# Kernel optimization log

Measured on AMD Instinct MI355X. Metric: run time of the kernel, lower is better.

The kernel has to match this reference:

```python
import jax, jax.numpy as jnp
import numpy as np

N = 100000          # nodes
E = 1600000         # edges (avg degree 16)
D_IN = 128          # in_features
D_OUT = 128         # out_features


def setup_inputs() -> dict:
    key = jax.random.key(0)
    k1, k2, k3, k4 = jax.random.split(key, 4)
    H = jax.random.normal(k1, (N, D_IN), dtype=jnp.float32)
    # COO indices of sparse adjacency A: row i aggregates features of col j
    src = jax.random.randint(k2, (E,), 0, N, dtype=jnp.int32)
    dst = jax.random.randint(k3, (E,), 0, N, dtype=jnp.int32)
    # nn.Linear(2*in_features, out_features): weight [out, 2*in], zero bias
    W = jax.random.normal(k4, (D_OUT, 2 * D_IN), dtype=jnp.float32) * 0.05
    b = jnp.zeros((D_OUT,), dtype=jnp.float32)
    return {"H": H, "src": src, "dst": dst, "W": W, "b": b}


def reference(H, src, dst, W, b):
    # max-aggregation: for each node i, max over features of its neighbors.
    # One fused gather + segment-max replaces the per-node Python loop.
    gathered = H[dst]  # [E, D_IN]
    agg = jax.ops.segment_max(gathered, src, num_segments=N)  # [N, D_IN]
    # nodes with no incoming edges stay zero (torch code leaves zeros)
    deg = jax.ops.segment_sum(jnp.ones((src.shape[0],), jnp.float32), src,
                              num_segments=N)  # [N]
    H_neigh = jnp.where(deg[:, None] > 0, agg, 0.0)
    H_concat = jnp.concatenate([H, H_neigh], axis=1)  # [N, 2*D_IN]
    return H_concat @ W.T + b
```

## Files before the change

kernel.cpp:

```cpp
#include <hip/hip_runtime.h>
#include <math.h>

#define NN 100000
#define NE 1600000
#define DD 128
#define NB 1563
#define CAP 1280
#define PB 391
#define CB 391

#define WS_HH  0
#define WS_CUR 6400000
#define WS_ENT (WS_CUR + NB)
#define WS_AH  (WS_ENT + NB * CAP)

typedef __attribute__((ext_vector_type(8))) _Float16 h8_t;
typedef __attribute__((ext_vector_type(4))) _Float16 h4_t;
typedef __attribute__((ext_vector_type(2))) _Float16 h2_t;
typedef __attribute__((ext_vector_type(4))) float f4_t;

__device__ __forceinline__ unsigned pk2h(float x, float y) {
    h2_t h;
    h.x = (_Float16)x;
    h.y = (_Float16)y;
    return *(unsigned*)&h;
}

__device__ __forceinline__ h4_t h4max(h4_t a, h4_t b) {
    return __builtin_elementwise_max(a, b);
}

__global__ __launch_bounds__(512) void prep_kernel(const float* __restrict__ H,
                                                   const int* __restrict__ src,
                                                   const int* __restrict__ dst,
                                                   int* __restrict__ cursor,
                                                   unsigned* __restrict__ entries,
                                                   uint4* __restrict__ Hh4) {
    __shared__ int cnt[NB];
    __shared__ int gcur[NB];
    const int t = threadIdx.x;
    const int b = blockIdx.x;
    if (b < PB) {
        for (int i = t; i < NB; i += 512) cnt[i] = 0;
        __syncthreads();
        const int base = b * 4096;
        int sv[8];
#pragma unroll
        for (int k = 0; k < 8; ++k) {
            int e = base + k * 512 + t;
            sv[k] = (e < NE) ? src[e] : -1;
            if (sv[k] >= 0) atomicAdd(&cnt[sv[k] >> 6], 1);
        }
        __syncthreads();
        for (int i = t; i < NB; i += 512) {
            int c = cnt[i];
            gcur[i] = c ? i * CAP + atomicAdd(&cursor[i], c) : 0;
        }
        __syncthreads();
#pragma unroll
        for (int k = 0; k < 8; ++k) {
            int e = base + k * 512 + t;
            if (sv[k] >= 0) {
                int s = sv[k];
                int pos = atomicAdd(&gcur[s >> 6], 1);
                entries[pos] = ((unsigned)(s & 63) << 17) | (unsigned)dst[e];
            }
        }
    } else {
        const int nb = b - PB;
        const int n8 = NN * DD / 8;
        for (int i = nb * 512 + t; i < n8; i += CB * 512) {
            const float4* s = (const float4*)H + (size_t)i * 2;
            float4 a = s[0], c4 = s[1];
            uint4 o;
            o.x = pk2h(a.x, a.y);
            o.y = pk2h(a.z, a.w);
            o.z = pk2h(c4.x, c4.y);
            o.w = pk2h(c4.z, c4.w);
            Hh4[i] = o;
        }
    }
}

__global__ __launch_bounds__(256) void agg_kernel(const _Float16* __restrict__ Hh,
                                                  const int* __restrict__ cursor,
                                                  const unsigned* __restrict__ entries,
                                                  unsigned* __restrict__ Ah) {
    __shared__ unsigned raw[CAP];
    __shared__ unsigned sorted[CAP];
    __shared__ int cnt[64], base_s[64], cur[64];
    const int t = threadIdx.x;
    const int b = blockIdx.x;
    const int n = cursor[b];

    if (t < 64) cnt[t] = 0;
    __syncthreads();
    for (int i = t; i < n; i += 256) {
        unsigned e = entries[b * CAP + i];
        raw[i] = e;
        atomicAdd(&cnt[e >> 17], 1);
    }
    __syncthreads();
    if (t < 64) {
        int v = cnt[t];
        int incl = v;
#pragma unroll
        for (int o = 1; o < 64; o <<= 1) {
            int y = __shfl_up(incl, o, 64);
            if (t >= o) incl += y;
        }
        base_s[t] = incl - v;
        cur[t] = incl - v;
    }
    __syncthreads();
    for (int i = t; i < n; i += 256) {
        unsigned e = raw[i];
        int pos = atomicAdd(&cur[e >> 17], 1);
        sorted[pos] = e & 0x1FFFFu;
    }
    __syncthreads();

    const int lane = t & 63;
    const int w = t >> 6;
    const int half = lane >> 5;
    const int l32 = lane & 31;
    const _Float16* __restrict__ colbase = Hh + l32 * 4;
#pragma unroll
    for (int q = 0; q < 16; ++q) {
        int ln = w * 16 + q;
        int s0 = base_s[ln];
        int e0 = s0 + cnt[ln];
        unsigned long long mu = 0xFC00FC00FC00FC00ull;
        h4_t m = *(h4_t*)&mu;
        int j = s0 + half;
        for (; j + 6 < e0; j += 8) {
            int d0 = sorted[j], d1 = sorted[j + 2];
            int d2 = sorted[j + 4], d3 = sorted[j + 6];
            h4_t v0 = *(const h4_t*)(colbase + (size_t)d0 * DD);
            h4_t v1 = *(const h4_t*)(colbase + (size_t)d1 * DD);
            h4_t v2 = *(const h4_t*)(colbase + (size_t)d2 * DD);
            h4_t v3 = *(const h4_t*)(colbase + (size_t)d3 * DD);
            m = h4max(m, h4max(h4max(v0, v1), h4max(v2, v3)));
        }
        for (; j < e0; j += 2) {
            h4_t v0 = *(const h4_t*)(colbase + (size_t)sorted[j] * DD);
            m = h4max(m, v0);
        }
        uint2 mv = *(uint2*)&m;
        uint2 ov;
        ov.x = (unsigned)__shfl_xor((int)mv.x, 32, 64);
        ov.y = (unsigned)__shfl_xor((int)mv.y, 32, 64);
        h4_t om = *(h4_t*)&ov;
        m = h4max(m, om);
        int node = b * 64 + ln;
        if (half == 0 && node < NN) {
            uint2 outv = make_uint2(0u, 0u);
            if (s0 < e0) outv = *(uint2*)&m;
            *(uint2*)(Ah + (size_t)node * 64 + l32 * 2) = outv;
        }
    }
}

#define XP 72
__global__ __launch_bounds__(256) void mfma_matmul_kernel(
        const unsigned short* __restrict__ Hh,
        const unsigned short* __restrict__ Ah,
        const float* __restrict__ W,
        const float* __restrict__ bias,
        float* __restrict__ out) {
    __shared__ unsigned short Xs[64 * XP];
    __shared__ unsigned short Ws[128 * XP];
    const int t = threadIdx.x;
    const int lane = t & 63;
    const int w = t >> 6;
    const int quad = lane >> 4;
    const int l16 = lane & 15;
    const int blockrow = blockIdx.x * 64;

    f4_t acc[8] = {};

    for (int c = 0; c < 4; ++c) {
        const int k0 = c * 64;
        {
            const unsigned short* xb = (c < 2) ? Hh : Ah;
            const int koff = (c < 2) ? k0 : k0 - 128;
            int seg = t & 7, r0 = t >> 3;
#pragma unroll
            for (int j = 0; j < 2; ++j) {
                int r = r0 + 32 * j;
                int row = blockrow + r;
                uint4 v = make_uint4(0, 0, 0, 0);
                if (row < NN)
                    v = *(const uint4*)(xb + (size_t)row * DD + koff + seg * 8);
                *(uint4*)&Xs[r * XP + seg * 8] = v;
            }
        }
        {
            int seg = t & 15, o0 = t >> 4;
#pragma unroll
            for (int j = 0; j < 8; ++j) {
                int o = o0 + 16 * j;
                float4 wv = *(const float4*)(W + (size_t)o * 256 + k0 + seg * 4);
                uint2 p;
                p.x = pk2h(wv.x, wv.y);
                p.y = pk2h(wv.z, wv.w);
                *(uint2*)&Ws[o * XP + seg * 4] = p;
            }
        }
        __syncthreads();
#pragma unroll
        for (int kk = 0; kk < 64; kk += 32) {
            h8_t a = *(const h8_t*)&Xs[(w * 16 + l16) * XP + kk + quad * 8];
#pragma unroll
            for (int ot = 0; ot < 8; ++ot) {
                h8_t bf = *(const h8_t*)&Ws[(ot * 16 + l16) * XP + kk + quad * 8];
                acc[ot] = __builtin_amdgcn_mfma_f32_16x16x32_f16(a, bf, acc[ot], 0, 0, 0);
            }
        }
        __syncthreads();
    }

#pragma unroll
    for (int ot = 0; ot < 8; ++ot) {
        float bv = bias[ot * 16 + l16];
#pragma unroll
        for (int reg = 0; reg < 4; ++reg) {
            int row = blockrow + w * 16 + quad * 4 + reg;
            if (row < NN)
                out[(size_t)row * DD + ot * 16 + l16] = acc[ot][reg] + bv;
        }
    }
}

extern "C" void kernel_launch(void* const* d_in, const int* in_sizes, int n_in,
                              void* d_out, int out_size, void* d_ws, size_t ws_size,
                              hipStream_t stream) {
    const float* H   = (const float*)d_in[0];
    const int*   src = (const int*)d_in[1];
    const int*   dst = (const int*)d_in[2];
    const float* W   = (const float*)d_in[3];
    const float* b   = (const float*)d_in[4];
    float* out = (float*)d_out;

    int* ws = (int*)d_ws;
    unsigned short* Hh      = (unsigned short*)(ws + WS_HH);
    int*            cursor  = ws + WS_CUR;
    unsigned*       entries = (unsigned*)(ws + WS_ENT);
    unsigned*       Ah      = (unsigned*)(ws + WS_AH);

    hipMemsetAsync(cursor, 0, NB * sizeof(int), stream);
    prep_kernel<<<PB + CB, 512, 0, stream>>>(H, src, dst, cursor, entries, (uint4*)Hh);
    agg_kernel<<<NB, 256, 0, stream>>>((const _Float16*)Hh, cursor, entries, Ah);
    mfma_matmul_kernel<<<(NN + 63) / 64, 256, 0, stream>>>(
        Hh, (const unsigned short*)Ah, W, b, out);
}
```

Before: 245.0 us.

## Pre-convert W to fp16 once, enlarge matmul row tile, widen prep blocks

```diff
diff --git a/kernel.cpp b/kernel.cpp
--- a/kernel.cpp
+++ b/kernel.cpp
@@ -6,13 +6,14 @@
 #define DD 128
 #define NB 1563
 #define CAP 1280
-#define PB 391
-#define CB 391
+#define PB 196
+#define CB 196
 
 #define WS_HH  0
 #define WS_CUR 6400000
 #define WS_ENT (WS_CUR + NB)
 #define WS_AH  (WS_ENT + NB * CAP)
+#define WS_WH  (WS_AH + NN * (DD / 2))
 
 typedef __attribute__((ext_vector_type(8))) _Float16 h8_t;
 typedef __attribute__((ext_vector_type(4))) _Float16 h4_t;
@@ -30,36 +31,45 @@
     return __builtin_elementwise_max(a, b);
 }
 
-__global__ __launch_bounds__(512) void prep_kernel(const float* __restrict__ H,
-                                                   const int* __restrict__ src,
-                                                   const int* __restrict__ dst,
-                                                   int* __restrict__ cursor,
-                                                   unsigned* __restrict__ entries,
-                                                   uint4* __restrict__ Hh4) {
+__global__ __launch_bounds__(1024) void init_kernel(const float* __restrict__ W,
+                                                    unsigned* __restrict__ Wh,
+                                                    int* __restrict__ cursor) {
+    int i = blockIdx.x * 1024 + threadIdx.x;
+    if (i < 128 * 256 / 2) Wh[i] = pk2h(W[2 * i], W[2 * i + 1]);
+    int j = i - 128 * 256 / 2;
+    if (j >= 0 && j < NB) cursor[j] = 0;
+}
+
+__global__ __launch_bounds__(1024) void prep_kernel(const float* __restrict__ H,
+                                                    const int* __restrict__ src,
+                                                    const int* __restrict__ dst,
+                                                    int* __restrict__ cursor,
+                                                    unsigned* __restrict__ entries,
+                                                    uint4* __restrict__ Hh4) {
     __shared__ int cnt[NB];
     __shared__ int gcur[NB];
     const int t = threadIdx.x;
     const int b = blockIdx.x;
     if (b < PB) {
-        for (int i = t; i < NB; i += 512) cnt[i] = 0;
-        __syncthreads();
-        const int base = b * 4096;
+        for (int i = t; i < NB; i += 1024) cnt[i] = 0;
+        __syncthreads();
+        const int base = b * 8192;
         int sv[8];
 #pragma unroll
         for (int k = 0; k < 8; ++k) {
-            int e = base + k * 512 + t;
+            int e = base + k * 1024 + t;
             sv[k] = (e < NE) ? src[e] : -1;
             if (sv[k] >= 0) atomicAdd(&cnt[sv[k] >> 6], 1);
         }
         __syncthreads();
-        for (int i = t; i < NB; i += 512) {
+        for (int i = t; i < NB; i += 1024) {
             int c = cnt[i];
             gcur[i] = c ? i * CAP + atomicAdd(&cursor[i], c) : 0;
         }
         __syncthreads();
 #pragma unroll
         for (int k = 0; k < 8; ++k) {
-            int e = base + k * 512 + t;
+            int e = base + k * 1024 + t;
             if (sv[k] >= 0) {
                 int s = sv[k];
                 int pos = atomicAdd(&gcur[s >> 6], 1);
@@ -69,7 +79,7 @@
     } else {
         const int nb = b - PB;
         const int n8 = NN * DD / 8;
-        for (int i = nb * 512 + t; i < n8; i += CB * 512) {
+        for (int i = nb * 1024 + t; i < n8; i += CB * 1024) {
             const float4* s = (const float4*)H + (size_t)i * 2;
             float4 a = s[0], c4 = s[1];
             uint4 o;
@@ -165,28 +175,28 @@
 __global__ __launch_bounds__(256) void mfma_matmul_kernel(
         const unsigned short* __restrict__ Hh,
         const unsigned short* __restrict__ Ah,
-        const float* __restrict__ W,
+        const unsigned short* __restrict__ Wh,
         const float* __restrict__ bias,
         float* __restrict__ out) {
-    __shared__ unsigned short Xs[64 * XP];
+    __shared__ unsigned short Xs[128 * XP];
     __shared__ unsigned short Ws[128 * XP];
     const int t = threadIdx.x;
     const int lane = t & 63;
     const int w = t >> 6;
     const int quad = lane >> 4;
     const int l16 = lane & 15;
-    const int blockrow = blockIdx.x * 64;
-
-    f4_t acc[8] = {};
+    const int blockrow = blockIdx.x * 128;
+
+    f4_t acc[2][8] = {};
 
     for (int c = 0; c < 4; ++c) {
         const int k0 = c * 64;
         {
             const unsigned short* xb = (c < 2) ? Hh : Ah;
             const int koff = (c < 2) ? k0 : k0 - 128;
-            int seg = t & 7, r0 = t >> 3;
-#pragma unroll
-            for (int j = 0; j < 2; ++j) {
+            const int seg = t & 7, r0 = t >> 3;
+#pragma unroll
+            for (int j = 0; j < 4; ++j) {
                 int r = r0 + 32 * j;
                 int row = blockrow + r;
                 uint4 v = make_uint4(0, 0, 0, 0);
@@ -196,25 +206,24 @@
             }
         }
         {
-            int seg = t & 15, o0 = t >> 4;
-#pragma unroll
-            for (int j = 0; j < 8; ++j) {
-                int o = o0 + 16 * j;
-                float4 wv = *(const float4*)(W + (size_t)o * 256 + k0 + seg * 4);
-                uint2 p;
-                p.x = pk2h(wv.x, wv.y);
-                p.y = pk2h(wv.z, wv.w);
-                *(uint2*)&Ws[o * XP + seg * 4] = p;
+            const int seg = t & 7, o0 = t >> 3;
+#pragma unroll
+            for (int j = 0; j < 4; ++j) {
+                int o = o0 + 32 * j;
+                uint4 v = *(const uint4*)(Wh + (size_t)o * 256 + k0 + seg * 8);
+                *(uint4*)&Ws[o * XP + seg * 8] = v;
             }
         }
         __syncthreads();
 #pragma unroll
         for (int kk = 0; kk < 64; kk += 32) {
-            h8_t a = *(const h8_t*)&Xs[(w * 16 + l16) * XP + kk + quad * 8];
+            h8_t a0 = *(const h8_t*)&Xs[(w * 32 + l16) * XP + kk + quad * 8];
+            h8_t a1 = *(const h8_t*)&Xs[(w * 32 + 16 + l16) * XP + kk + quad * 8];
 #pragma unroll
             for (int ot = 0; ot < 8; ++ot) {
                 h8_t bf = *(const h8_t*)&Ws[(ot * 16 + l16) * XP + kk + quad * 8];
-                acc[ot] = __builtin_amdgcn_mfma_f32_16x16x32_f16(a, bf, acc[ot], 0, 0, 0);
+                acc[0][ot] = __builtin_amdgcn_mfma_f32_16x16x32_f16(a0, bf, acc[0][ot], 0, 0, 0);
+                acc[1][ot] = __builtin_amdgcn_mfma_f32_16x16x32_f16(a1, bf, acc[1][ot], 0, 0, 0);
             }
         }
         __syncthreads();
@@ -224,10 +233,13 @@
     for (int ot = 0; ot < 8; ++ot) {
         float bv = bias[ot * 16 + l16];
 #pragma unroll
-        for (int reg = 0; reg < 4; ++reg) {
-            int row = blockrow + w * 16 + quad * 4 + reg;
-            if (row < NN)
-                out[(size_t)row * DD + ot * 16 + l16] = acc[ot][reg] + bv;
+        for (int sub = 0; sub < 2; ++sub) {
+#pragma unroll
+            for (int reg = 0; reg < 4; ++reg) {
+                int row = blockrow + w * 32 + sub * 16 + quad * 4 + reg;
+                if (row < NN)
+                    out[(size_t)row * DD + ot * 16 + l16] = acc[sub][ot][reg] + bv;
+            }
         }
     }
 }
@@ -247,10 +259,11 @@
     int*            cursor  = ws + WS_CUR;
     unsigned*       entries = (unsigned*)(ws + WS_ENT);
     unsigned*       Ah      = (unsigned*)(ws + WS_AH);
-
-    hipMemsetAsync(cursor, 0, NB * sizeof(int), stream);
-    prep_kernel<<<PB + CB, 512, 0, stream>>>(H, src, dst, cursor, entries, (uint4*)Hh);
+    unsigned*       Wh      = (unsigned*)(ws + WS_WH);
+
+    init_kernel<<<18, 1024, 0, stream>>>(W, Wh, cursor);
+    prep_kernel<<<PB + CB, 1024, 0, stream>>>(H, src, dst, cursor, entries, (uint4*)Hh);
     agg_kernel<<<NB, 256, 0, stream>>>((const _Float16*)Hh, cursor, entries, Ah);
-    mfma_matmul_kernel<<<(NN + 63) / 64, 256, 0, stream>>>(
-        Hh, (const unsigned short*)Ah, W, b, out);
-}
+    mfma_matmul_kernel<<<(NN + 127) / 128, 256, 0, stream>>>(
+        Hh, (const unsigned short*)Ah, (const unsigned short*)Wh, b, out);
+}
```

Result: faster. 238.3 us (-2.7%).
